# Optimization experiments

Hardware: AMD Instinct MI355X
Metric: run time of the kernel (lower is better)

The kernel has to match this reference:

```python
import jax, jax.numpy as jnp
import numpy as np

B, T, H, M, S, E, IN = 8, 2048, 64, 32, 20, 3, 32
EPS = 1e-8  # torch CosineSimilarity eps


def setup_inputs() -> dict:
    key = jax.random.key(0)
    ks = jax.random.split(key, 7)
    return {
        "x": jax.random.normal(ks[0], (B, T, IN), jnp.float32),
        "hidden": jax.random.normal(ks[1], (E, B, T, H), jnp.float32),
        "memory": jax.random.normal(ks[2], (S, M), jnp.float32),
        "Wq": jax.random.normal(ks[3], (E, H, M), jnp.float32),
        "Wk": jax.random.normal(ks[4], (E, H, M), jnp.float32),
        "Wv": jax.random.normal(ks[5], (E, H, M), jnp.float32),
        "input_query": jax.random.normal(ks[6], (IN, M), jnp.float32),
    }


def _cosine(a, b):
    # torch.nn.CosineSimilarity(dim=-1): each vector norm clamped to eps
    na = jnp.maximum(jnp.linalg.norm(a, axis=-1), EPS)
    nb = jnp.maximum(jnp.linalg.norm(b, axis=-1), EPS)
    return jnp.sum(a * b, axis=-1) / (na * nb)


def reference(x, hidden, memory, Wq, Wk, Wv, input_query):
    # query_mem: soft read from global memory slots
    q_in = jnp.einsum('bti,im->btm', x, input_query)           # [B,T,M]
    mem_sc = jax.nn.softmax(jnp.einsum('btm,sm->bts', q_in, memory), axis=-1)
    memories = jnp.einsum('bts,sm->btm', mem_sc, memory)       # [B,T,M]

    # per-expert tiny self-attention (vectorized over expert axis e)
    Q = jnp.einsum('ebth,ehm->ebtm', hidden, Wq)
    K = jnp.einsum('ebth,ehm->ebtm', hidden, Wk)
    V = jnp.einsum('ebth,ehm->ebtm', hidden, Wv)
    energy = jnp.einsum('ebtm,ebsm->ebts', Q, K)               # [E,B,T,T]
    att = jax.nn.softmax(energy, axis=-1)
    out = jnp.einsum('ebts,ebsm->ebtm', att, V)                # [E,B,T,M]

    cos = _cosine(memories[None], out)                         # [E,B,T]
    return jnp.moveaxis(cos, 0, -1)                            # [B,T,E]
```

## Files before the change

kernel.cpp:

```cpp
#include <hip/hip_runtime.h>
#include <hip/hip_bf16.h>

#define Bv  8
#define Tv  2048
#define Hv  64
#define Mv  32
#define Sv  20
#define Ev  3
#define INv 32
#define LOG2E 1.44269504088896340736f

typedef __attribute__((ext_vector_type(8))) _Float16 half8;
typedef __attribute__((ext_vector_type(2))) __fp16 fp16x2;
typedef __attribute__((ext_vector_type(4))) float float4v;

__device__ __forceinline__ void split2x4(float4 a, float4 b, half8& h, half8& l) {
    float vv[8] = {a.x, a.y, a.z, a.w, b.x, b.y, b.z, b.w};
#pragma unroll
    for (int i = 0; i < 8; ++i) {
        _Float16 hh = (_Float16)vv[i];
        h[i] = hh;
        l[i] = (_Float16)(vv[i] - (float)hh);
    }
}

__global__ __launch_bounds__(256) void qkv_kernel(
    const float* __restrict__ hidden,
    const float* __restrict__ Wq,
    const float* __restrict__ Wk,
    const float* __restrict__ Wv,
    const float* __restrict__ x,
    const float* __restrict__ memory,
    const float* __restrict__ iq,
    _Float16* __restrict__ Qh, _Float16* __restrict__ Ql,
    _Float16* __restrict__ Kh, _Float16* __restrict__ Kl,
    _Float16* __restrict__ Vth,
    float* __restrict__ memout)
{
    __shared__ __align__(16) char sBlob[24576];
    __shared__ float sIQ[32][32];
    __shared__ float sM[20][32];

    int bid  = blockIdx.x;
    int tile = bid & 31;
    int b    = (bid >> 5) & 7;
    int e    = bid >> 8;
    int tid  = threadIdx.x;
    int lane = tid & 63;
    int w    = tid >> 6;
    int quad = lane >> 4;
    int l15  = lane & 15;
    size_t eb = (size_t)(e * Bv + b);
    size_t row0 = eb * Tv + (size_t)tile * 64;
    const float* hbase = hidden + row0 * Hv;

    const float* arow = hbase + (size_t)(w * 16 + l15) * Hv + quad * 8;
    float4 a0 = *(const float4*)(arow);
    float4 a1 = *(const float4*)(arow + 4);
    float4 a2 = *(const float4*)(arow + 32);
    float4 a3 = *(const float4*)(arow + 36);

    if (e == 0) {
        for (int i = tid; i < 32 * 32; i += 256) sIQ[i >> 5][i & 31] = iq[i];
        for (int i = tid; i < 20 * 32; i += 256) sM[i >> 5][i & 31] = memory[i];
    }

    {
        const float* wsrc[3] = {Wq + (size_t)e * Hv * Mv,
                                Wk + (size_t)e * Hv * Mv,
                                Wv + (size_t)e * Hv * Mv};
#pragma unroll
        for (int j = 0; j < 3; ++j) {
            int u  = tid + j * 256;
            int c  = u >> 3, kb = u & 7;
            const float* src = wsrc[c >> 5] + (c & 31);
            float scale = (c < 32) ? LOG2E : 1.f;
            half8 hi, lo;
#pragma unroll
            for (int i = 0; i < 8; ++i) {
                float v = src[(kb * 8 + i) * Mv] * scale;
                _Float16 hh = (_Float16)v;
                hi[i] = hh;
                lo[i] = (_Float16)(v - (float)hh);
            }
            int off = c * 128 + ((kb ^ (c & 7)) << 4);
            *(half8*)(sBlob + off)         = hi;
            *(half8*)(sBlob + 12288 + off) = lo;
        }
    }

    half8 aH0, aL0, aH1, aL1;
    split2x4(a0, a1, aH0, aL0);
    split2x4(a2, a3, aH1, aL1);

    __syncthreads();

    float4v accs[6];
    int x7 = l15 & 7;
#pragma unroll
    for (int ct = 0; ct < 6; ++ct) {
        const char* brow = sBlob + (ct * 16 + l15) * 128;
        half8 bH0 = *(const half8*)(brow + ((quad ^ x7) << 4));
        half8 bH1 = *(const half8*)(brow + (((4 + quad) ^ x7) << 4));
        half8 bL0 = *(const half8*)(brow + 12288 + ((quad ^ x7) << 4));
        half8 bL1 = *(const half8*)(brow + 12288 + (((4 + quad) ^ x7) << 4));
        float4v acc = {0.f, 0.f, 0.f, 0.f};
        acc = __builtin_amdgcn_mfma_f32_16x16x32_f16(aH0, bL0, acc, 0, 0, 0);
        acc = __builtin_amdgcn_mfma_f32_16x16x32_f16(aL0, bH0, acc, 0, 0, 0);
        acc = __builtin_amdgcn_mfma_f32_16x16x32_f16(aH0, bH0, acc, 0, 0, 0);
        acc = __builtin_amdgcn_mfma_f32_16x16x32_f16(aH1, bL1, acc, 0, 0, 0);
        acc = __builtin_amdgcn_mfma_f32_16x16x32_f16(aL1, bH1, acc, 0, 0, 0);
        acc = __builtin_amdgcn_mfma_f32_16x16x32_f16(aH1, bH1, acc, 0, 0, 0);
        accs[ct] = acc;
    }

    __syncthreads();

    char* sQh = sBlob;
    char* sQl = sBlob + 4096;
    char* sKh = sBlob + 8192;
    char* sKl = sBlob + 12288;
    char* sVh = sBlob + 16384;
    int rbase = w * 16 + quad * 4;
#pragma unroll
    for (int ct = 0; ct < 6; ++ct) {
        int c = ct * 16 + l15;
#pragma unroll
        for (int r = 0; r < 4; ++r) {
            int row = rbase + r;
            float v = accs[ct][r];
            if (ct < 2) {
                _Float16 h16 = (_Float16)v;
                *(_Float16*)(sQh + row * 64 + c * 2) = h16;
                *(_Float16*)(sQl + row * 64 + c * 2) = (_Float16)(v - (float)h16);
            } else if (ct < 4) {
                _Float16 h16 = (_Float16)v;
                int m = c - 32, q = m >> 3, wi = m & 7;
                int off = row * 64 + (((q + row) & 3) << 4) + wi * 2;
                *(_Float16*)(sKh + off) = h16;
                *(_Float16*)(sKl + off) = (_Float16)(v - (float)h16);
            } else {
                int d = c - 64, c8 = row >> 3, wi = row & 7;
                int off = d * 128 + (((c8 + d) & 7) << 4) + wi * 2;
                *(_Float16*)(sVh + off) = (_Float16)v;
            }
        }
    }
    __syncthreads();

    size_t pb = eb * (size_t)Tv * 32 + (size_t)tile * 2048;
    _Float16* dsts[5] = {Qh + pb, Ql + pb, Kh + pb, Kl + pb, Vth + pb};
#pragma unroll
    for (int pl = 0; pl < 5; ++pl)
        ((float4*)dsts[pl])[tid] = ((const float4*)(sBlob + pl * 4096))[tid];

    if (e == 0 && tid < 64) {
        int t = b * Tv + tile * 64 + tid;
        const float4* xr = (const float4*)(x + (size_t)t * INv);
        float xv[32];
#pragma unroll
        for (int i = 0; i < 8; ++i) {
            float4 v = xr[i];
            xv[4*i] = v.x; xv[4*i+1] = v.y; xv[4*i+2] = v.z; xv[4*i+3] = v.w;
        }
        float qm[32];
#pragma unroll
        for (int m = 0; m < 32; ++m) qm[m] = 0.f;
        for (int i = 0; i < 32; ++i) {
            float xi = xv[i];
#pragma unroll
            for (int m4 = 0; m4 < 8; ++m4) {
                float4 wv = *(const float4*)&sIQ[i][m4 * 4];
                qm[4*m4]   = fmaf(xi, wv.x, qm[4*m4]);
                qm[4*m4+1] = fmaf(xi, wv.y, qm[4*m4+1]);
                qm[4*m4+2] = fmaf(xi, wv.z, qm[4*m4+2]);
                qm[4*m4+3] = fmaf(xi, wv.w, qm[4*m4+3]);
            }
        }
        float sc[20];
#pragma unroll
        for (int j = 0; j < 20; ++j) {
            float a2 = 0.f;
#pragma unroll
            for (int m = 0; m < 32; ++m) a2 = fmaf(qm[m], sM[j][m], a2);
            sc[j] = a2;
        }
        float mx = sc[0];
#pragma unroll
        for (int j = 1; j < 20; ++j) mx = fmaxf(mx, sc[j]);
        float psum = 0.f, p[20];
#pragma unroll
        for (int j = 0; j < 20; ++j) { p[j] = exp2f((sc[j] - mx) * LOG2E); psum += p[j]; }
        float inv = 1.0f / psum;
        float mo[32];
#pragma unroll
        for (int m = 0; m < 32; ++m) mo[m] = 0.f;
        for (int j = 0; j < 20; ++j) {
            float pj = p[j];
#pragma unroll
            for (int m = 0; m < 32; ++m) mo[m] = fmaf(pj, sM[j][m], mo[m]);
        }
        float4* outp = (float4*)(memout + (size_t)t * Mv);
#pragma unroll
        for (int m4 = 0; m4 < 8; ++m4) {
            float4 v;
            v.x = mo[4*m4] * inv; v.y = mo[4*m4+1] * inv;
            v.z = mo[4*m4+2] * inv; v.w = mo[4*m4+3] * inv;
            outp[m4] = v;
        }
    }
}

__device__ __forceinline__ void load_lds16(const _Float16* g, char* l) {
    __builtin_amdgcn_global_load_lds(
        (const __attribute__((address_space(1))) void*)g,
        (__attribute__((address_space(3))) void*)l, 16, 0, 0);
}

__global__ __launch_bounds__(256, 1) void attn_kernel(
    const _Float16* __restrict__ Qh, const _Float16* __restrict__ Ql,
    const _Float16* __restrict__ Kh, const _Float16* __restrict__ Kl,
    const _Float16* __restrict__ Vth,
    const float* __restrict__ memv,
    float* __restrict__ out)
{
    __shared__ __align__(16) char smem[32768];
    const int PW = 24576;

    int bid  = blockIdx.x;
    int xcd  = bid & 7;
    int slot = bid >> 3;
    int tile = slot & 31;
    int ebi  = xcd + ((slot >> 5) << 3);
    int e    = ebi >> 3;
    int b    = ebi & 7;
    int tid  = threadIdx.x;
    int lane = tid & 63;
    int w    = tid >> 6;
    int quad = lane >> 4;
    int l15  = lane & 15;
    size_t eb = (size_t)ebi;
    int q0 = tile * 64 + w * 16;

    size_t qoff = (eb * Tv + (size_t)(q0 + l15)) * 32 + quad * 8;
    half8 qH = *(const half8*)(Qh + qoff);
    half8 qL = *(const half8*)(Ql + qoff);

    float4v O0 = {0.f, 0.f, 0.f, 0.f};
    float4v O1 = {0.f, 0.f, 0.f, 0.f};
    float m_run = -3.0e38f;

    size_t ebOff = eb * (size_t)Tv * 32;
    const _Float16* gp[3] = {Kh + ebOff, Kl + ebOff, Vth + ebOff};

#pragma unroll
    for (int j = 0; j < 3; ++j) {
        int idx = w * 3 + j, p = idx >> 2, k = idx & 3;
        load_lds16(gp[p] + (size_t)k * 512 + lane * 8,
                   smem + p * 4096 + k * 1024);
    }

    for (int c = 0; c < 32; ++c) {
        int pb = c & 1;
        __syncthreads();
        if (c + 1 < 32) {
#pragma unroll
            for (int j = 0; j < 3; ++j) {
                int idx = w * 3 + j, p = idx >> 2, k = idx & 3;
                load_lds16(gp[p] + (size_t)(c + 1) * 2048 + k * 512 + lane * 8,
                           smem + (pb ^ 1) * 12288 + p * 4096 + k * 1024);
            }
        }
        const char* base = smem + pb * 12288;

        float s[16];
        float cmax = -3.0e38f;
#pragma unroll
        for (int tau = 0; tau < 4; ++tau) {
            int r = tau * 16 + l15;
            int sw = ((quad + r) & 3) << 4;
            half8 aH = *(const half8*)(base + r * 64 + sw);
            half8 aL = *(const half8*)(base + 4096 + r * 64 + sw);
            float4v acc = {0.f, 0.f, 0.f, 0.f};
            acc = __builtin_amdgcn_mfma_f32_16x16x32_f16(aH, qL, acc, 0, 0, 0);
            acc = __builtin_amdgcn_mfma_f32_16x16x32_f16(aL, qH, acc, 0, 0, 0);
            acc = __builtin_amdgcn_mfma_f32_16x16x32_f16(aH, qH, acc, 0, 0, 0);
#pragma unroll
            for (int r2 = 0; r2 < 4; ++r2) {
                s[tau * 4 + r2] = acc[r2];
                cmax = fmaxf(cmax, acc[r2]);
            }
        }
        cmax = fmaxf(cmax, __shfl_xor(cmax, 16));
        cmax = fmaxf(cmax, __shfl_xor(cmax, 32));
        float mNew  = fmaxf(m_run, cmax);
        float alpha = exp2f(m_run - mNew);
#pragma unroll
        for (int i = 0; i < 16; ++i)
            s[i] = exp2f(s[i] - mNew);
        m_run = mNew;

#pragma unroll
        for (int r = 0; r < 4; ++r) {
            float ar = __shfl(alpha, quad * 4 + r, 16);
            O0[r] *= ar;
            O1[r] *= ar;
        }

        char* pw = smem + PW + w * 2048 + l15 * 128;
        int xr = l15 & 7;
#pragma unroll
        for (int tau = 0; tau < 4; ++tau) {
            fp16x2 h01 = __builtin_amdgcn_cvt_pkrtz(s[tau*4+0], s[tau*4+1]);
            fp16x2 h23 = __builtin_amdgcn_cvt_pkrtz(s[tau*4+2], s[tau*4+3]);
            uint2 u;
            u.x = __builtin_bit_cast(unsigned int, h01);
            u.y = __builtin_bit_cast(unsigned int, h23);
            int bi = tau * 2 + (quad >> 1);
            *(uint2*)(pw + ((bi ^ xr) << 4) + (quad & 1) * 8) = u;
        }
        __asm__ volatile("" ::: "memory");

#pragma unroll
        for (int ks = 0; ks < 2; ++ks) {
            int swv = ((ks * 4 + quad + l15) & 7) << 4;
            half8 pA  = *(const half8*)(pw + (((ks * 4 + quad) ^ xr) << 4));
            half8 v0H = *(const half8*)(base + 8192 + l15 * 128 + swv);
            half8 v1H = *(const half8*)(base + 8192 + (16 + l15) * 128 + swv);
            O0 = __builtin_amdgcn_mfma_f32_16x16x32_f16(pA, v0H, O0, 0, 0, 0);
            O1 = __builtin_amdgcn_mfma_f32_16x16x32_f16(pA, v1H, O1, 0, 0, 0);
        }
    }

    const float* mb = memv + (size_t)b * Tv * 32;
    float dotr[4], nor[4], nmr[4];
#pragma unroll
    for (int r = 0; r < 4; ++r) {
        int trow = q0 + quad * 4 + r;
        float mv0 = mb[(size_t)trow * 32 + l15];
        float mv1 = mb[(size_t)trow * 32 + 16 + l15];
        float d  = O0[r] * mv0 + O1[r] * mv1;
        float n  = O0[r] * O0[r] + O1[r] * O1[r];
        float nm = mv0 * mv0 + mv1 * mv1;
#pragma unroll
        for (int delta = 1; delta < 16; delta <<= 1) {
            d  += __shfl_xor(d,  delta);
            n  += __shfl_xor(n,  delta);
            nm += __shfl_xor(nm, delta);
        }
        dotr[r] = d; nor[r] = n; nmr[r] = nm;
    }
    if (l15 < 4) {
        int r = l15;
        float na = fmaxf(sqrtf(nmr[r]), 1e-8f);
        float nb = fmaxf(sqrtf(nor[r]), 1e-30f);
        float cosv = dotr[r] / (na * nb);
        int trow = q0 + quad * 4 + r;
        out[((size_t)b * Tv + trow) * Ev + e] = cosv;
    }
}

extern "C" void kernel_launch(void* const* d_in, const int* in_sizes, int n_in,
                              void* d_out, int out_size, void* d_ws, size_t ws_size,
                              hipStream_t stream) {
    const float* x      = (const float*)d_in[0];
    const float* hidden = (const float*)d_in[1];
    const float* memory = (const float*)d_in[2];
    const float* Wq     = (const float*)d_in[3];
    const float* Wk     = (const float*)d_in[4];
    const float* Wv     = (const float*)d_in[5];
    const float* iq     = (const float*)d_in[6];
    float* out          = (float*)d_out;

    char* ws = (char*)d_ws;
    const size_t PLANE = (size_t)Ev * Bv * Tv * 32 * 2;
    float*    memout = (float*)ws;
    _Float16* Qh  = (_Float16*)(ws + 2097152);
    _Float16* Ql  = (_Float16*)(ws + 2097152 + PLANE);
    _Float16* Kh  = (_Float16*)(ws + 2097152 + 2 * PLANE);
    _Float16* Kl  = (_Float16*)(ws + 2097152 + 3 * PLANE);
    _Float16* Vth = (_Float16*)(ws + 2097152 + 4 * PLANE);

    qkv_kernel<<<Ev * Bv * (Tv / 64), 256, 0, stream>>>(hidden, Wq, Wk, Wv,
                                                        x, memory, iq,
                                                        Qh, Ql, Kh, Kl, Vth, memout);
    attn_kernel<<<Ev * Bv * (Tv / 64), 256, 0, stream>>>(Qh, Ql, Kh, Kl, Vth,
                                                         memout, out);
}
```

Before: 146.0 us.

## Split keys across waves with register-resident K/V and lazy softmax rescaling

The attention kernel now gives each wave a quarter of the key range and all 64 queries of the tile. K/V fragments are loaded straight from global memory into registers, double-buffered in software, which replaces the LDS staging and per-chunk barriers. Partial softmax states are merged through shared memory at the end. The running max is only updated when a new score exceeds it by more than 8 (log2 domain), which skips most rescales. The score result is reused as the B operand of 16x16x16 MFMAs, so P no longer round-trips through LDS. The cost is more registers for four query tiles, a larger final reduction, unswizzled layouts in the QKV producer, and a risk of fp16 overflow in P from the lazy max threshold.

```diff
diff --git a/kernel.cpp b/kernel.cpp
--- a/kernel.cpp
+++ b/kernel.cpp
@@ -11,18 +11,9 @@
 #define LOG2E 1.44269504088896340736f
 
 typedef __attribute__((ext_vector_type(8))) _Float16 half8;
+typedef __attribute__((ext_vector_type(4))) _Float16 half4v;
 typedef __attribute__((ext_vector_type(2))) __fp16 fp16x2;
 typedef __attribute__((ext_vector_type(4))) float float4v;
-
-__device__ __forceinline__ void split2x4(float4 a, float4 b, half8& h, half8& l) {
-    float vv[8] = {a.x, a.y, a.z, a.w, b.x, b.y, b.z, b.w};
-#pragma unroll
-    for (int i = 0; i < 8; ++i) {
-        _Float16 hh = (_Float16)vv[i];
-        h[i] = hh;
-        l[i] = (_Float16)(vv[i] - (float)hh);
-    }
-}
 
 __global__ __launch_bounds__(256) void qkv_kernel(
     const float* __restrict__ hidden,
@@ -90,8 +81,20 @@
     }
 
     half8 aH0, aL0, aH1, aL1;
-    split2x4(a0, a1, aH0, aL0);
-    split2x4(a2, a3, aH1, aL1);
+    {
+        float vv[8] = {a0.x, a0.y, a0.z, a0.w, a1.x, a1.y, a1.z, a1.w};
+#pragma unroll
+        for (int i = 0; i < 8; ++i) {
+            _Float16 hh = (_Float16)vv[i];
+            aH0[i] = hh; aL0[i] = (_Float16)(vv[i] - (float)hh);
+        }
+        float ww[8] = {a2.x, a2.y, a2.z, a2.w, a3.x, a3.y, a3.z, a3.w};
+#pragma unroll
+        for (int i = 0; i < 8; ++i) {
+            _Float16 hh = (_Float16)ww[i];
+            aH1[i] = hh; aL1[i] = (_Float16)(ww[i] - (float)hh);
+        }
+    }
 
     __syncthreads();
 
@@ -135,13 +138,13 @@
                 *(_Float16*)(sQl + row * 64 + c * 2) = (_Float16)(v - (float)h16);
             } else if (ct < 4) {
                 _Float16 h16 = (_Float16)v;
-                int m = c - 32, q = m >> 3, wi = m & 7;
-                int off = row * 64 + (((q + row) & 3) << 4) + wi * 2;
+                int m = c - 32;
+                int off = row * 64 + m * 2;
                 *(_Float16*)(sKh + off) = h16;
                 *(_Float16*)(sKl + off) = (_Float16)(v - (float)h16);
             } else {
-                int d = c - 64, c8 = row >> 3, wi = row & 7;
-                int off = d * 128 + (((c8 + d) & 7) << 4) + wi * 2;
+                int d = c - 64;
+                int off = d * 128 + row * 2;
                 *(_Float16*)(sVh + off) = (_Float16)v;
             }
         }
@@ -211,21 +214,59 @@
     }
 }
 
-__device__ __forceinline__ void load_lds16(const _Float16* g, char* l) {
-    __builtin_amdgcn_global_load_lds(
-        (const __attribute__((address_space(1))) void*)g,
-        (__attribute__((address_space(3))) void*)l, 16, 0, 0);
-}
-
-__global__ __launch_bounds__(256, 1) void attn_kernel(
+#define ATT_LOAD(c, KH, KL, V0, V1)                                           \
+    {                                                                         \
+        size_t ko = ebOff + (size_t)((c) * 64 + w * 16 + l15) * 32 + quad * 8;\
+        KH = *(const half8*)(Kh + ko);                                        \
+        KL = *(const half8*)(Kl + ko);                                        \
+        size_t vo = ebOff + (size_t)(c) * 2048 + (size_t)l15 * 64             \
+                    + w * 16 + quad * 4;                                      \
+        V0 = *(const half4v*)(Vth + vo);                                      \
+        V1 = *(const half4v*)(Vth + vo + 1024);                               \
+    }
+
+#define ATT_BODY(KH, KL, V0, V1)                                              \
+    _Pragma("unroll")                                                         \
+    for (int qt = 0; qt < 4; ++qt) {                                          \
+        float4v acc = {0.f, 0.f, 0.f, 0.f};                                   \
+        acc = __builtin_amdgcn_mfma_f32_16x16x32_f16(KH, qL[qt], acc, 0,0,0); \
+        acc = __builtin_amdgcn_mfma_f32_16x16x32_f16(KL, qH[qt], acc, 0,0,0); \
+        acc = __builtin_amdgcn_mfma_f32_16x16x32_f16(KH, qH[qt], acc, 0,0,0); \
+        float pmax = fmaxf(fmaxf(acc[0], acc[1]), fmaxf(acc[2], acc[3]));     \
+        pmax = fmaxf(pmax, __shfl_xor(pmax, 16));                             \
+        pmax = fmaxf(pmax, __shfl_xor(pmax, 32));                             \
+        if (__any(pmax > mm[qt] + 8.0f)) {                                    \
+            float mn = fmaxf(mm[qt], pmax);                                   \
+            float al = exp2f(mm[qt] - mn);                                    \
+            mm[qt] = mn;                                                      \
+            _Pragma("unroll")                                                 \
+            for (int r = 0; r < 4; ++r) {                                     \
+                O[qt][0][r] *= al; O[qt][1][r] *= al;                         \
+            }                                                                 \
+        }                                                                     \
+        fp16x2 p01 = __builtin_amdgcn_cvt_pkrtz(exp2f(acc[0] - mm[qt]),       \
+                                                exp2f(acc[1] - mm[qt]));      \
+        fp16x2 p23 = __builtin_amdgcn_cvt_pkrtz(exp2f(acc[2] - mm[qt]),       \
+                                                exp2f(acc[3] - mm[qt]));      \
+        unsigned long long up =                                               \
+            ((unsigned long long)__builtin_bit_cast(unsigned int, p23) << 32) \
+            | __builtin_bit_cast(unsigned int, p01);                          \
+        half4v pB = __builtin_bit_cast(half4v, up);                           \
+        O[qt][0] = __builtin_amdgcn_mfma_f32_16x16x16f16(V0, pB, O[qt][0],    \
+                                                         0, 0, 0);            \
+        O[qt][1] = __builtin_amdgcn_mfma_f32_16x16x16f16(V1, pB, O[qt][1],    \
+                                                         0, 0, 0);            \
+    }
+
+__global__ __launch_bounds__(256, 3) void attn_kernel(
     const _Float16* __restrict__ Qh, const _Float16* __restrict__ Ql,
     const _Float16* __restrict__ Kh, const _Float16* __restrict__ Kl,
     const _Float16* __restrict__ Vth,
     const float* __restrict__ memv,
     float* __restrict__ out)
 {
-    __shared__ __align__(16) char smem[32768];
-    const int PW = 24576;
+    __shared__ float sO[4][64][33];
+    __shared__ float sMw[4][64];
 
     int bid  = blockIdx.x;
     int xcd  = bid & 7;
@@ -240,123 +281,72 @@
     int quad = lane >> 4;
     int l15  = lane & 15;
     size_t eb = (size_t)ebi;
-    int q0 = tile * 64 + w * 16;
-
-    size_t qoff = (eb * Tv + (size_t)(q0 + l15)) * 32 + quad * 8;
-    half8 qH = *(const half8*)(Qh + qoff);
-    half8 qL = *(const half8*)(Ql + qoff);
-
-    float4v O0 = {0.f, 0.f, 0.f, 0.f};
-    float4v O1 = {0.f, 0.f, 0.f, 0.f};
-    float m_run = -3.0e38f;
-
     size_t ebOff = eb * (size_t)Tv * 32;
-    const _Float16* gp[3] = {Kh + ebOff, Kl + ebOff, Vth + ebOff};
-
-#pragma unroll
-    for (int j = 0; j < 3; ++j) {
-        int idx = w * 3 + j, p = idx >> 2, k = idx & 3;
-        load_lds16(gp[p] + (size_t)k * 512 + lane * 8,
-                   smem + p * 4096 + k * 1024);
-    }
-
-    for (int c = 0; c < 32; ++c) {
-        int pb = c & 1;
-        __syncthreads();
-        if (c + 1 < 32) {
-#pragma unroll
-            for (int j = 0; j < 3; ++j) {
-                int idx = w * 3 + j, p = idx >> 2, k = idx & 3;
-                load_lds16(gp[p] + (size_t)(c + 1) * 2048 + k * 512 + lane * 8,
-                           smem + (pb ^ 1) * 12288 + p * 4096 + k * 1024);
-            }
-        }
-        const char* base = smem + pb * 12288;
-
-        float s[16];
-        float cmax = -3.0e38f;
-#pragma unroll
-        for (int tau = 0; tau < 4; ++tau) {
-            int r = tau * 16 + l15;
-            int sw = ((quad + r) & 3) << 4;
-            half8 aH = *(const half8*)(base + r * 64 + sw);
-            half8 aL = *(const half8*)(base + 4096 + r * 64 + sw);
-            float4v acc = {0.f, 0.f, 0.f, 0.f};
-            acc = __builtin_amdgcn_mfma_f32_16x16x32_f16(aH, qL, acc, 0, 0, 0);
-            acc = __builtin_amdgcn_mfma_f32_16x16x32_f16(aL, qH, acc, 0, 0, 0);
-            acc = __builtin_amdgcn_mfma_f32_16x16x32_f16(aH, qH, acc, 0, 0, 0);
-#pragma unroll
-            for (int r2 = 0; r2 < 4; ++r2) {
-                s[tau * 4 + r2] = acc[r2];
-                cmax = fmaxf(cmax, acc[r2]);
-            }
-        }
-        cmax = fmaxf(cmax, __shfl_xor(cmax, 16));
-        cmax = fmaxf(cmax, __shfl_xor(cmax, 32));
-        float mNew  = fmaxf(m_run, cmax);
-        float alpha = exp2f(m_run - mNew);
-#pragma unroll
-        for (int i = 0; i < 16; ++i)
-            s[i] = exp2f(s[i] - mNew);
-        m_run = mNew;
-
-#pragma unroll
-        for (int r = 0; r < 4; ++r) {
-            float ar = __shfl(alpha, quad * 4 + r, 16);
-            O0[r] *= ar;
-            O1[r] *= ar;
-        }
-
-        char* pw = smem + PW + w * 2048 + l15 * 128;
-        int xr = l15 & 7;
-#pragma unroll
-        for (int tau = 0; tau < 4; ++tau) {
-            fp16x2 h01 = __builtin_amdgcn_cvt_pkrtz(s[tau*4+0], s[tau*4+1]);
-            fp16x2 h23 = __builtin_amdgcn_cvt_pkrtz(s[tau*4+2], s[tau*4+3]);
-            uint2 u;
-            u.x = __builtin_bit_cast(unsigned int, h01);
-            u.y = __builtin_bit_cast(unsigned int, h23);
-            int bi = tau * 2 + (quad >> 1);
-            *(uint2*)(pw + ((bi ^ xr) << 4) + (quad & 1) * 8) = u;
-        }
-        __asm__ volatile("" ::: "memory");
-
-#pragma unroll
-        for (int ks = 0; ks < 2; ++ks) {
-            int swv = ((ks * 4 + quad + l15) & 7) << 4;
-            half8 pA  = *(const half8*)(pw + (((ks * 4 + quad) ^ xr) << 4));
-            half8 v0H = *(const half8*)(base + 8192 + l15 * 128 + swv);
-            half8 v1H = *(const half8*)(base + 8192 + (16 + l15) * 128 + swv);
-            O0 = __builtin_amdgcn_mfma_f32_16x16x32_f16(pA, v0H, O0, 0, 0, 0);
-            O1 = __builtin_amdgcn_mfma_f32_16x16x32_f16(pA, v1H, O1, 0, 0, 0);
-        }
-    }
-
-    const float* mb = memv + (size_t)b * Tv * 32;
-    float dotr[4], nor[4], nmr[4];
-#pragma unroll
-    for (int r = 0; r < 4; ++r) {
-        int trow = q0 + quad * 4 + r;
-        float mv0 = mb[(size_t)trow * 32 + l15];
-        float mv1 = mb[(size_t)trow * 32 + 16 + l15];
-        float d  = O0[r] * mv0 + O1[r] * mv1;
-        float n  = O0[r] * O0[r] + O1[r] * O1[r];
-        float nm = mv0 * mv0 + mv1 * mv1;
-#pragma unroll
-        for (int delta = 1; delta < 16; delta <<= 1) {
-            d  += __shfl_xor(d,  delta);
-            n  += __shfl_xor(n,  delta);
-            nm += __shfl_xor(nm, delta);
-        }
-        dotr[r] = d; nor[r] = n; nmr[r] = nm;
-    }
-    if (l15 < 4) {
-        int r = l15;
-        float na = fmaxf(sqrtf(nmr[r]), 1e-8f);
-        float nb = fmaxf(sqrtf(nor[r]), 1e-30f);
-        float cosv = dotr[r] / (na * nb);
-        int trow = q0 + quad * 4 + r;
-        out[((size_t)b * Tv + trow) * Ev + e] = cosv;
+
+    half8 qH[4], qL[4];
+#pragma unroll
+    for (int qt = 0; qt < 4; ++qt) {
+        size_t qoff = ebOff + (size_t)(tile * 64 + qt * 16 + l15) * 32 + quad * 8;
+        qH[qt] = *(const half8*)(Qh + qoff);
+        qL[qt] = *(const half8*)(Ql + qoff);
+    }
+
+    float4v O[4][2];
+#pragma unroll
+    for (int qt = 0; qt < 4; ++qt) {
+        O[qt][0] = {0.f, 0.f, 0.f, 0.f};
+        O[qt][1] = {0.f, 0.f, 0.f, 0.f};
+    }
+    float mm[4] = {-3.0e38f, -3.0e38f, -3.0e38f, -3.0e38f};
+
+    half8 kHa, kLa, kHb, kLb;
+    half4v v0a, v1a, v0b, v1b;
+    ATT_LOAD(0, kHa, kLa, v0a, v1a);
+
+    for (int c = 0; c < 32; c += 2) {
+        ATT_LOAD(c + 1, kHb, kLb, v0b, v1b);
+        ATT_BODY(kHa, kLa, v0a, v1a);
+        if (c + 2 < 32) ATT_LOAD(c + 2, kHa, kLa, v0a, v1a);
+        ATT_BODY(kHb, kLb, v0b, v1b);
+    }
+
+#pragma unroll
+    for (int qt = 0; qt < 4; ++qt) {
+        int q = qt * 16 + l15;
+        sMw[w][q] = mm[qt];
+#pragma unroll
+        for (int dh = 0; dh < 2; ++dh)
+#pragma unroll
+            for (int r = 0; r < 4; ++r)
+                sO[w][q][dh * 16 + quad * 4 + r] = O[qt][dh][r];
+    }
+    __syncthreads();
+
+    int q  = tid >> 2;
+    int dq = tid & 3;
+    float ms0 = sMw[0][q], ms1 = sMw[1][q], ms2 = sMw[2][q], ms3 = sMw[3][q];
+    float M  = fmaxf(fmaxf(ms0, ms1), fmaxf(ms2, ms3));
+    float g0 = exp2f(ms0 - M), g1 = exp2f(ms1 - M);
+    float g2 = exp2f(ms2 - M), g3 = exp2f(ms3 - M);
+    const float* mb = memv + ((size_t)b * Tv + tile * 64 + q) * 32 + dq * 8;
+    float dotm = 0.f, oo = 0.f, mm2 = 0.f;
+#pragma unroll
+    for (int j = 0; j < 8; ++j) {
+        int d = dq * 8 + j;
+        float o = g0 * sO[0][q][d] + g1 * sO[1][q][d]
+                + g2 * sO[2][q][d] + g3 * sO[3][q][d];
+        float mvv = mb[j];
+        dotm = fmaf(o, mvv, dotm);
+        oo   = fmaf(o, o, oo);
+        mm2  = fmaf(mvv, mvv, mm2);
+    }
+    dotm += __shfl_xor(dotm, 1); dotm += __shfl_xor(dotm, 2);
+    oo   += __shfl_xor(oo, 1);   oo   += __shfl_xor(oo, 2);
+    mm2  += __shfl_xor(mm2, 1);  mm2  += __shfl_xor(mm2, 2);
+    if (dq == 0) {
+        float na = fmaxf(sqrtf(mm2), 1e-8f);
+        float nb = fmaxf(sqrtf(oo), 1e-30f);
+        out[((size_t)b * Tv + tile * 64 + q) * Ev + e] = dotm / (na * nb);
     }
 }
 
```

Result: no change. 147.5 us (+1.0%).
